# Performance work log

Hardware: AMD Instinct MI355X
Metric: run time of the kernel (lower is better)

Reference implementation:

```python
import jax, jax.numpy as jnp
import numpy as np

B, C, H, W = 1024, 3, 32, 32
NCLS = 10

def _conv(x, w, b, padding):
    y = jax.lax.conv_general_dilated(x, w, (1, 1), padding, dimension_numbers=('NCHW', 'OIHW', 'NCHW'))
    return y + b[None, :, None, None]

def _maxpool2(x):
    return jax.lax.reduce_window(x, -jnp.inf, jax.lax.max, (1, 1, 2, 2), (1, 1, 2, 2), 'VALID')

def _lenet(x, lw1, lb1, lw2, lb2, lfc1, lfb1, lfc2, lfb2, lfc3, lfb3):
    h = jax.nn.relu(_conv(x, lw1, lb1, 'VALID'))   # [B,6,28,28]
    h = _maxpool2(h)                               # [B,6,14,14]
    h = jax.nn.relu(_conv(h, lw2, lb2, 'VALID'))   # [B,16,10,10]
    h = _maxpool2(h)                               # [B,16,5,5]
    h = h.reshape(h.shape[0], -1)                  # [B,400]
    h = jax.nn.relu(h @ lfc1 + lfb1)
    h = jax.nn.relu(h @ lfc2 + lfb2)
    return h @ lfc3 + lfb3                         # [B,10]

def _resnet(x, rw0, rb0, rw1a, rb1a, rw1b, rb1b, rw2a, rb2a, rw2b, rb2b, rfc, rfb):
    h = jax.nn.relu(_conv(x, rw0, rb0, 'SAME'))    # [B,64,32,32]
    r = jax.nn.relu(_conv(h, rw1a, rb1a, 'SAME'))
    r = _conv(r, rw1b, rb1b, 'SAME')
    h = jax.nn.relu(h + r)
    r = jax.nn.relu(_conv(h, rw2a, rb2a, 'SAME'))
    r = _conv(r, rw2b, rb2b, 'SAME')
    h = jax.nn.relu(h + r)
    h = h.mean(axis=(2, 3))                        # [B,64]
    return h @ rfc + rfb                           # [B,10]

def setup_inputs():
    key = jax.random.key(0)
    ks = jax.random.split(key, 16)
    def w(k, shape, fan_in):
        return jax.random.normal(k, shape, jnp.float32) * np.float32(1.0 / np.sqrt(fan_in))
    return {
        'x': jax.random.normal(ks[0], (B, C, H, W), jnp.float32),
        'threshold': jnp.float32(0.3),
        'labels': jax.random.randint(ks[1], (B,), 0, NCLS),
        'lw1': w(ks[2], (6, 3, 5, 5), 75), 'lb1': jnp.zeros((6,), jnp.float32),
        'lw2': w(ks[3], (16, 6, 5, 5), 150), 'lb2': jnp.zeros((16,), jnp.float32),
        'lfc1': w(ks[4], (400, 120), 400), 'lfb1': jnp.zeros((120,), jnp.float32),
        'lfc2': w(ks[5], (120, 84), 120), 'lfb2': jnp.zeros((84,), jnp.float32),
        'lfc3': w(ks[6], (84, NCLS), 84), 'lfb3': jnp.zeros((NCLS,), jnp.float32),
        'rw0': w(ks[7], (64, 3, 3, 3), 27), 'rb0': jnp.zeros((64,), jnp.float32),
        'rw1a': w(ks[8], (64, 64, 3, 3), 576), 'rb1a': jnp.zeros((64,), jnp.float32),
        'rw1b': w(ks[9], (64, 64, 3, 3), 576), 'rb1b': jnp.zeros((64,), jnp.float32),
        'rw2a': w(ks[10], (64, 64, 3, 3), 576), 'rb2a': jnp.zeros((64,), jnp.float32),
        'rw2b': w(ks[11], (64, 64, 3, 3), 576), 'rb2b': jnp.zeros((64,), jnp.float32),
        'rfc': w(ks[12], (64, NCLS), 64), 'rfb': jnp.zeros((NCLS,), jnp.float32),
    }

def reference(x, threshold, labels, lw1, lb1, lw2, lb2, lfc1, lfb1, lfc2, lfb2, lfc3, lfb3, rw0, rb0, rw1a, rb1a, rw1b, rb1b, rw2a, rb2a, rw2b, rb2b, rfc, rfb):
    out = _lenet(x, lw1, lb1, lw2, lb2, lfc1, lfb1, lfc2, lfb2, lfc3, lfb3)
    pred = jnp.argmax(out, axis=1)
    # fused confusion-matrix update: single scatter-add replaces the 10x10 python loop
    conf_matrix = jnp.zeros((NCLS, NCLS), jnp.float32).at[labels, pred].add(1.0)
    probs = jax.nn.softmax(out, axis=1)
    top2, _ = jax.lax.top_k(probs, 2)
    low_conf = (top2[:, 0] - top2[:, 1]) <= threshold    # [B] bool
    # batched fallback: one grouped resnet call + masked merge replaces the per-sample loop
    res_out = _resnet(x, rw0, rb0, rw1a, rb1a, rw1b, rb1b, rw2a, rb2a, rw2b, rb2b, rfc, rfb)
    out = jnp.where(low_conf[:, None], res_out, out)
    return out, conf_matrix
```

## Files before the change

### kernel.cpp

```cpp
#include <hip/hip_runtime.h>
#include <hip/hip_bf16.h>
#include <math.h>

#define BATCH 1024

typedef __attribute__((ext_vector_type(8))) short bf16x8;
typedef __attribute__((ext_vector_type(4))) float f32x4;

#define IMG_ELEMS 73984
#define IMG_B 147968
#define ROW_B 4352
#define CH_B 544
#define WT_OFF 43520
#define WT_HALF_B 36864

__global__ __launch_bounds__(256) void lenet_conv1(const float* __restrict__ x,
    const float* __restrict__ w, const float* __restrict__ bias, float* __restrict__ p1)
{
    __shared__ float img[3 * 1024];
    __shared__ float wl[450];
    __shared__ float bl[6];
    int b = blockIdx.x, t = threadIdx.x;
    for (int i = t; i < 3072; i += 256) img[i] = x[(size_t)b * 3072 + i];
    for (int i = t; i < 450; i += 256) wl[i] = w[i];
    if (t < 6) bl[t] = bias[t];
    __syncthreads();
    for (int idx = t; idx < 1176; idx += 256) {
        int o = idx / 196, r = idx - o * 196, py = r / 14, px = r - py * 14;
        int y0 = 2 * py, x0 = 2 * px;
        float s00, s01, s10, s11;
        s00 = s01 = s10 = s11 = bl[o];
        for (int c = 0; c < 3; c++) {
            float pv[6][6];
            #pragma unroll
            for (int i2 = 0; i2 < 6; i2++)
                #pragma unroll
                for (int j2 = 0; j2 < 6; j2++)
                    pv[i2][j2] = img[c * 1024 + (y0 + i2) * 32 + x0 + j2];
            const float* wc = &wl[o * 75 + c * 25];
            #pragma unroll
            for (int ky = 0; ky < 5; ky++)
                #pragma unroll
                for (int kx = 0; kx < 5; kx++) {
                    float wv = wc[ky * 5 + kx];
                    s00 += pv[ky][kx] * wv;
                    s01 += pv[ky][kx + 1] * wv;
                    s10 += pv[ky + 1][kx] * wv;
                    s11 += pv[ky + 1][kx + 1] * wv;
                }
        }
        float m = fmaxf(fmaxf(s00, s01), fmaxf(s10, s11));
        p1[(size_t)b * 1176 + idx] = fmaxf(m, 0.f);
    }
}

__global__ __launch_bounds__(256) void lenet_conv2(const float* __restrict__ p1,
    const float* __restrict__ w, const float* __restrict__ bias, float* __restrict__ p2)
{
    __shared__ float img[1176];
    __shared__ float wl[2400];
    __shared__ float bl[16];
    int b = blockIdx.x, t = threadIdx.x;
    for (int i = t; i < 1176; i += 256) img[i] = p1[(size_t)b * 1176 + i];
    for (int i = t; i < 2400; i += 256) wl[i] = w[i];
    if (t < 16) bl[t] = bias[t];
    __syncthreads();
    for (int idx = t; idx < 400; idx += 256) {
        int o = idx / 25, r = idx - o * 25, py = r / 5, px = r - py * 5;
        int y0 = 2 * py, x0 = 2 * px;
        float s00, s01, s10, s11;
        s00 = s01 = s10 = s11 = bl[o];
        for (int c = 0; c < 6; c++) {
            float pv[6][6];
            #pragma unroll
            for (int i2 = 0; i2 < 6; i2++)
                #pragma unroll
                for (int j2 = 0; j2 < 6; j2++)
                    pv[i2][j2] = img[c * 196 + (y0 + i2) * 14 + x0 + j2];
            const float* wc = &wl[o * 150 + c * 25];
            #pragma unroll
            for (int ky = 0; ky < 5; ky++)
                #pragma unroll
                for (int kx = 0; kx < 5; kx++) {
                    float wv = wc[ky * 5 + kx];
                    s00 += pv[ky][kx] * wv;
                    s01 += pv[ky][kx + 1] * wv;
                    s10 += pv[ky + 1][kx] * wv;
                    s11 += pv[ky + 1][kx + 1] * wv;
                }
        }
        float m = fmaxf(fmaxf(s00, s01), fmaxf(s10, s11));
        p2[(size_t)b * 400 + idx] = fmaxf(m, 0.f);
    }
}

__global__ __launch_bounds__(256) void lenet_fc(const float* __restrict__ p2,
    const float* __restrict__ w1, const float* __restrict__ b1,
    const float* __restrict__ w2, const float* __restrict__ b2,
    const float* __restrict__ w3, const float* __restrict__ b3,
    const int* __restrict__ labels, const float* __restrict__ thr,
    float* __restrict__ out, float* __restrict__ conf, int* __restrict__ flags)
{
    __shared__ float xin[400];
    __shared__ float h1[120];
    __shared__ float h2[84];
    __shared__ float ps[256];
    __shared__ float lg[10];
    int b = blockIdx.x, t = threadIdx.x;
    for (int i = t; i < 400; i += 256) xin[i] = p2[(size_t)b * 400 + i];
    __syncthreads();
    {
        int n = t & 127, half = t >> 7;
        float s = 0.f;
        if (n < 120) {
            int k0 = half * 200;
            for (int k = k0; k < k0 + 200; k++) s += xin[k] * w1[k * 120 + n];
        }
        ps[t] = s;
    }
    __syncthreads();
    if (t < 120) h1[t] = fmaxf(ps[t] + ps[t + 128] + b1[t], 0.f);
    __syncthreads();
    {
        int n = t & 127, half = t >> 7;
        float s = 0.f;
        if (n < 84) {
            int k0 = half * 60;
            for (int k = k0; k < k0 + 60; k++) s += h1[k] * w2[k * 84 + n];
        }
        ps[t] = s;
    }
    __syncthreads();
    if (t < 84) h2[t] = fmaxf(ps[t] + ps[t + 128] + b2[t], 0.f);
    __syncthreads();
    if (t < 10) {
        float s = b3[t];
        for (int k = 0; k < 84; k++) s += h2[k] * w3[k * 10 + t];
        lg[t] = s;
        out[(size_t)b * 10 + t] = s;
    }
    __syncthreads();
    if (t == 0) {
        int pred = 0;
        float m = lg[0];
        #pragma unroll
        for (int j = 1; j < 10; j++) if (lg[j] > m) { m = lg[j]; pred = j; }
        float se = 0.f, m2 = -1e30f;
        #pragma unroll
        for (int j = 0; j < 10; j++) {
            se += expf(lg[j] - m);
            if (j != pred) m2 = fmaxf(m2, lg[j]);
        }
        float gap = (1.f - expf(m2 - m)) / se;
        flags[b] = (gap <= thr[0]) ? 1 : 0;
        atomicAdd(&conf[labels[b] * 10 + pred], 1.f);
    }
}

__global__ __launch_bounds__(256) void prep_weights(
    const float* __restrict__ w0, const float* __restrict__ w1,
    const float* __restrict__ w2, const float* __restrict__ w3,
    __hip_bfloat16* __restrict__ dst)
{
    int tid = blockIdx.x * 256 + threadIdx.x;
    if (tid >= 4 * 36864) return;
    int c = tid / 36864, r = tid - c * 36864;
    int tap = r / 4096, r2 = r - tap * 4096;
    int co = r2 >> 6, ci = r2 & 63;
    const float* src = (c == 0) ? w0 : (c == 1) ? w1 : (c == 2) ? w2 : w3;
    float v = src[((size_t)co * 64 + ci) * 9 + tap];
    int nh = co >> 5, nt = (co >> 4) & 1, m = co & 15;
    int kb = ci >> 5, q = (ci >> 3) & 3, e = ci & 7;
    size_t elem = (size_t)(c * 2 + nh) * 18432
                + (size_t)((tap * 2 + kb) * 2 + nt) * 512 + q * 128 + m * 8 + e;
    dst[elem] = __float2bfloat16(v);
}

__global__ __launch_bounds__(256) void prep_w0t(const float* __restrict__ w,
                                                float* __restrict__ dst)
{
    int tid = blockIdx.x * 256 + threadIdx.x;
    if (tid >= 1728) return;
    int k = tid >> 6, co = tid & 63;
    dst[tid] = w[co * 27 + k];
}

__global__ __launch_bounds__(256) void zero_borders(__hip_bfloat16* __restrict__ buf, int cb)
{
    int tid = blockIdx.x * 256 + threadIdx.x;
    int total = cb * 132 * 8;
    if (tid >= total) return;
    int img = tid / 1056, r = tid - img * 1056;
    int pxi = r >> 3, chunk = r & 7;
    int row, col;
    if (pxi < 34)       { row = 0;  col = pxi; }
    else if (pxi < 68)  { row = 33; col = pxi - 34; }
    else if (pxi < 100) { row = pxi - 67; col = 0; }
    else                { row = pxi - 99; col = 33; }
    uint4 z = {0, 0, 0, 0};
    *(uint4*)((char*)buf + (size_t)img * IMG_B + (size_t)row * ROW_B
              + chunk * CH_B + col * 16) = z;
}

__global__ __launch_bounds__(256) void conv0_nhwc(const float* __restrict__ x,
    const float* __restrict__ wT, const float* __restrict__ bias,
    __hip_bfloat16* __restrict__ out, int cb)
{
    __shared__ char smem[8 * ROW_B];
    float* sl = (float*)smem;
    int bid = blockIdx.x;
    int img = bid % cb, strip = bid / cb;
    int r0 = strip * 8;
    int t = threadIdx.x;
    const float* xi = x + (size_t)img * 3072;
    for (int i = t; i < 1020; i += 256) {
        int c = i / 340, rr2 = i - c * 340;
        int rr = rr2 / 34, cc = rr2 - rr * 34;
        int y = r0 + rr - 1, xx = cc - 1;
        float v = 0.f;
        if (y >= 0 && y < 32 && xx >= 0 && xx < 32) v = xi[c * 1024 + y * 32 + xx];
        sl[(c * 10 + rr) * 34 + cc] = v;
    }
    __syncthreads();

    int rr = t >> 5, col = t & 31;
    float iv[27];
    #pragma unroll
    for (int c = 0; c < 3; c++)
        #pragma unroll
        for (int dy = 0; dy < 3; dy++)
            #pragma unroll
            for (int dx = 0; dx < 3; dx++)
                iv[c * 9 + dy * 3 + dx] = sl[(c * 10 + rr + dy) * 34 + col + dx];
    __syncthreads();

    float s[64];
    #pragma unroll
    for (int co = 0; co < 64; co++) s[co] = bias[co];
    #pragma unroll
    for (int k = 0; k < 27; k++) {
        const float v = iv[k];
        const float* wk = wT + k * 64;
        #pragma unroll
        for (int co = 0; co < 64; co++) s[co] = fmaf(v, wk[co], s[co]);
    }
    __hip_bfloat16 ov[64];
    #pragma unroll
    for (int co = 0; co < 64; co++) ov[co] = __float2bfloat16(fmaxf(s[co], 0.f));

    char* brow = smem + rr * ROW_B + (col + 1) * 16;
    const uint4* srcv = (const uint4*)ov;
    #pragma unroll
    for (int j = 0; j < 8; j++) *(uint4*)(brow + j * CH_B) = srcv[j];
    if (t < 128) {
        int row = t >> 4, ch = (t >> 1) & 7, side = t & 1;
        uint4 z = {0, 0, 0, 0};
        *(uint4*)(smem + row * ROW_B + ch * CH_B + (side ? 33 : 0) * 16) = z;
    }
    __syncthreads();
    char* gbase = (char*)out + (size_t)img * IMG_B + (size_t)(r0 + 1) * ROW_B;
    for (int u = t; u < 2176; u += 256)
        *(uint4*)(gbase + (size_t)u * 16) = *(const uint4*)(smem + (size_t)u * 16);
}

template<bool ADD>
__global__ __launch_bounds__(256, 2) void conv3x3_lds(
    const __hip_bfloat16* __restrict__ act, const __hip_bfloat16* __restrict__ wts,
    const float* __restrict__ bias, const __hip_bfloat16* __restrict__ skip,
    __hip_bfloat16* __restrict__ out, int cb)
{
    __shared__ char sl[WT_OFF + WT_HALF_B];
    int bid = blockIdx.x;
    int img = bid % cb;
    int rem = bid / cb;
    int strip = rem >> 1, nh = rem & 1;
    int t = threadIdx.x;
    int w = t >> 6, lane = t & 63;
    int m = lane & 15, q = lane >> 4;

    const char* gsrc = (const char*)act + (size_t)img * IMG_B + (size_t)(strip * 8) * ROW_B;
    for (int u0 = w * 64; u0 < 2720; u0 += 256) {
        int u = u0 + lane;
        if (u < 2720)
            __builtin_amdgcn_global_load_lds(
                (const __attribute__((address_space(1))) unsigned int*)(gsrc + (size_t)u * 16),
                (__attribute__((address_space(3))) unsigned int*)(sl + u0 * 16), 16, 0, 0);
    }
    const char* gw = (const char*)wts + (size_t)nh * WT_HALF_B;
    for (int u0 = w * 64; u0 < 2304; u0 += 256)
        __builtin_amdgcn_global_load_lds(
            (const __attribute__((address_space(1))) unsigned int*)(gw + (size_t)(u0 + lane) * 16),
            (__attribute__((address_space(3))) unsigned int*)(sl + WT_OFF + u0 * 16), 16, 0, 0);
    __syncthreads();

    int abase[4];
    #pragma unroll
    for (int mt = 0; mt < 4; mt++)
        abase[mt] = (2 * w + (mt >> 1)) * ROW_B + ((mt & 1) * 16 + m) * 16 + q * CH_B;
    int bbase[2];
    #pragma unroll
    for (int nt = 0; nt < 2; nt++)
        bbase[nt] = WT_OFF + nt * 1024 + q * 256 + m * 16;

    f32x4 acc[4][2] = {};
    bf16x8 a[2][4], b[2][2];

    #define ALOAD(s, buf)                                                      \
        {                                                                      \
            const int tap_ = (s) >> 1, kb_ = (s) & 1;                          \
            const int dy_ = tap_ / 3, dx_ = tap_ - dy_ * 3;                    \
            const int aoff_ = dy_ * ROW_B + kb_ * (4 * CH_B) + dx_ * 16;       \
            _Pragma("unroll")                                                  \
            for (int mt = 0; mt < 4; mt++)                                     \
                a[buf][mt] = *(const bf16x8*)(sl + abase[mt] + aoff_);         \
        }
    #define BLOAD(s, buf)                                                      \
        {                                                                      \
            const int boff_ = ((s) >> 1) * 4096 + ((s) & 1) * 2048;            \
            _Pragma("unroll")                                                  \
            for (int nt = 0; nt < 2; nt++)                                     \
                b[buf][nt] = *(const bf16x8*)(sl + bbase[nt] + boff_);         \
        }

    ALOAD(0, 0) BLOAD(0, 0)
    #pragma unroll
    for (int s = 0; s < 18; s++) {
        int cur = s & 1;
        if (s < 17) { ALOAD(s + 1, cur ^ 1) BLOAD(s + 1, cur ^ 1) }
        #pragma unroll
        for (int mt = 0; mt < 4; mt++)
            #pragma unroll
            for (int nt = 0; nt < 2; nt++)
                acc[mt][nt] = __builtin_amdgcn_mfma_f32_16x16x32_bf16(
                    a[cur][mt], b[cur][nt], acc[mt][nt], 0, 0, 0);
    }
    #undef ALOAD
    #undef BLOAD

    __syncthreads();
    #pragma unroll
    for (int nt = 0; nt < 2; nt++) {
        float bv = bias[nh * 32 + nt * 16 + m];
        #pragma unroll
        for (int mt = 0; mt < 4; mt++) {
            int pl = (2 * w + (mt >> 1)) * 32 + (mt & 1) * 16 + q * 4;
            #pragma unroll
            for (int r = 0; r < 4; r++) {
                __hip_bfloat16 hv = __float2bfloat16(acc[mt][nt][r] + bv);
                *(__hip_bfloat16*)(sl + (size_t)(pl + r) * 72 + (nt * 16 + m) * 2) = hv;
            }
        }
    }
    __syncthreads();

    char* oimg = (char*)out + (size_t)img * IMG_B;
    const char* simg = (const char*)skip + (size_t)img * IMG_B;
    int ch = (t >> 5) & 3, px = t & 31, rhalf = t >> 7;
    #pragma unroll
    for (int pass = 0; pass < 4; pass++) {
        int rl = pass * 2 + rhalf;
        size_t goff = (size_t)(strip * 8 + 1 + rl) * ROW_B + (nh * 4 + ch) * CH_B + (px + 1) * 16;
        bf16x8 v = *(const bf16x8*)(sl + (size_t)(rl * 32 + px) * 72 + ch * 16);
        bf16x8 o;
        if (ADD) {
            bf16x8 sv = *(const bf16x8*)(simg + goff);
            #pragma unroll
            for (int e = 0; e < 8; e++) {
                float f = __bfloat162float(((__hip_bfloat16*)&v)[e])
                        + __bfloat162float(((__hip_bfloat16*)&sv)[e]);
                ((__hip_bfloat16*)&o)[e] = __float2bfloat16(fmaxf(f, 0.f));
            }
        } else {
            #pragma unroll
            for (int e = 0; e < 8; e++) {
                float f = __bfloat162float(((__hip_bfloat16*)&v)[e]);
                ((__hip_bfloat16*)&o)[e] = __float2bfloat16(fmaxf(f, 0.f));
            }
        }
        *(bf16x8*)(oimg + goff) = o;
    }
}

__global__ __launch_bounds__(256) void res_head_bf16(const __hip_bfloat16* __restrict__ h,
    const float* __restrict__ rfc, const float* __restrict__ rfb,
    const int* __restrict__ flags, float* __restrict__ out)
{
    __shared__ float part[4][64];
    __shared__ float mns[64];
    int img = blockIdx.x, t = threadIdx.x;
    int w = t >> 6, lane = t & 63;
    int c = lane & 7;
    const char* base = (const char*)h + (size_t)img * IMG_B;

    float s8[8];
    #pragma unroll
    for (int j = 0; j < 8; j++) s8[j] = 0.f;

    for (int ry = 0; ry < 8; ry++) {
        int row = w * 8 + ry + 1;
        const char* rb = base + (size_t)row * ROW_B;
        #pragma unroll
        for (int k = 0; k < 4; k++) {
            int g = lane + 64 * k;
            bf16x8 v = *(const bf16x8*)(rb + c * CH_B + ((g >> 3) + 1) * 16);
            #pragma unroll
            for (int j = 0; j < 8; j++)
                s8[j] += __bfloat162float(*(__hip_bfloat16*)&((short*)&v)[j]);
        }
    }
    #pragma unroll
    for (int off = 8; off <= 32; off <<= 1)
        #pragma unroll
        for (int j = 0; j < 8; j++) s8[j] += __shfl_xor(s8[j], off, 64);
    if (lane < 8)
        #pragma unroll
        for (int j = 0; j < 8; j++) part[w][c * 8 + j] = s8[j];
    __syncthreads();
    if (t < 64) mns[t] = (part[0][t] + part[1][t] + part[2][t] + part[3][t]) * (1.f / 1024.f);
    __syncthreads();
    if (t < 10 && flags[img]) {
        float s2 = rfb[t];
        for (int cc = 0; cc < 64; cc++) s2 += mns[cc] * rfc[cc * 10 + t];
        out[(size_t)img * 10 + t] = s2;
    }
}

extern "C" void kernel_launch(void* const* d_in, const int* in_sizes, int n_in,
                              void* d_out, int out_size, void* d_ws, size_t ws_size,
                              hipStream_t stream)
{
    const float* x    = (const float*)d_in[0];
    const float* thr  = (const float*)d_in[1];
    const int*   labels = (const int*)d_in[2];
    const float* lw1 = (const float*)d_in[3];  const float* lb1 = (const float*)d_in[4];
    const float* lw2 = (const float*)d_in[5];  const float* lb2 = (const float*)d_in[6];
    const float* lfc1 = (const float*)d_in[7]; const float* lfb1 = (const float*)d_in[8];
    const float* lfc2 = (const float*)d_in[9]; const float* lfb2 = (const float*)d_in[10];
    const float* lfc3 = (const float*)d_in[11];const float* lfb3 = (const float*)d_in[12];
    const float* rw0 = (const float*)d_in[13]; const float* rb0 = (const float*)d_in[14];
    const float* rw1a = (const float*)d_in[15];const float* rb1a = (const float*)d_in[16];
    const float* rw1b = (const float*)d_in[17];const float* rb1b = (const float*)d_in[18];
    const float* rw2a = (const float*)d_in[19];const float* rb2a = (const float*)d_in[20];
    const float* rw2b = (const float*)d_in[21];const float* rb2b = (const float*)d_in[22];
    const float* rfc = (const float*)d_in[23]; const float* rfb = (const float*)d_in[24];

    float* out  = (float*)d_out;
    float* conf = out + (size_t)BATCH * 10;

    int nc = 1;
    while (nc < 16 &&
           2ull * (size_t)(BATCH / nc) * 147968ull + 294912ull + 16384ull > ws_size)
        nc <<= 1;
    int cb = BATCH / nc;

    __hip_bfloat16* A  = (__hip_bfloat16*)d_ws;
    __hip_bfloat16* Bb = A + (size_t)cb * IMG_ELEMS;
    __hip_bfloat16* wprep = Bb + (size_t)cb * IMG_ELEMS;
    int* flags = (int*)((char*)wprep + 294912);
    float* w0t = (float*)((char*)wprep + 294912 + 4096);

    float* p1 = (float*)A;
    float* p2 = p1 + 1204224;

    hipMemsetAsync(conf, 0, 100 * sizeof(float), stream);

    prep_weights<<<(4 * 36864 + 255) / 256, 256, 0, stream>>>(rw1a, rw1b, rw2a, rw2b, wprep);
    prep_w0t<<<7, 256, 0, stream>>>(rw0, w0t);

    lenet_conv1<<<BATCH, 256, 0, stream>>>(x, lw1, lb1, p1);
    lenet_conv2<<<BATCH, 256, 0, stream>>>(p1, lw2, lb2, p2);
    lenet_fc<<<BATCH, 256, 0, stream>>>(p2, lfc1, lfb1, lfc2, lfb2, lfc3, lfb3,
                                        labels, thr, out, conf, flags);

    int zb = (cb * 1056 + 255) / 256;
    zero_borders<<<zb, 256, 0, stream>>>(A, cb);
    zero_borders<<<zb, 256, 0, stream>>>(Bb, cb);

    const __hip_bfloat16* W1a = wprep;
    const __hip_bfloat16* W1b = wprep + 36864;
    const __hip_bfloat16* W2a = wprep + 2 * 36864;
    const __hip_bfloat16* W2b = wprep + 3 * 36864;

    for (int c0 = 0; c0 < BATCH; c0 += cb) {
        const float* xc = x + (size_t)c0 * 3072;
        conv0_nhwc<<<cb * 4, 256, 0, stream>>>(xc, w0t, rb0, A, cb);
        conv3x3_lds<false><<<cb * 8, 256, 0, stream>>>(A,  W1a, rb1a, nullptr, Bb, cb);
        conv3x3_lds<true ><<<cb * 8, 256, 0, stream>>>(Bb, W1b, rb1b, A, A, cb);
        conv3x3_lds<false><<<cb * 8, 256, 0, stream>>>(A,  W2a, rb2a, nullptr, Bb, cb);
        conv3x3_lds<true ><<<cb * 8, 256, 0, stream>>>(Bb, W2b, rb2b, A, A, cb);
        res_head_bf16<<<cb, 256, 0, stream>>>(A, rfc, rfb, flags + c0, out + (size_t)c0 * 10);
    }
}
```

Before: 702.9 us.

## Make conv3x3 blocks persistent over four row strips with prefetched halo

```diff
diff --git a/kernel.cpp b/kernel.cpp
--- a/kernel.cpp
+++ b/kernel.cpp
@@ -13,6 +13,8 @@
 #define CH_B 544
 #define WT_OFF 43520
 #define WT_HALF_B 36864
+#define BOUNCE_OFF 25088
+#define STAGE_A_U 1568
 
 __global__ __launch_bounds__(256) void lenet_conv1(const float* __restrict__ x,
     const float* __restrict__ w, const float* __restrict__ bias, float* __restrict__ p1)
@@ -263,6 +265,11 @@
         *(uint4*)(gbase + (size_t)u * 16) = *(const uint4*)(smem + (size_t)u * 16);
 }
 
+#define GLL(gp, lp)                                                            \
+    __builtin_amdgcn_global_load_lds(                                          \
+        (const __attribute__((address_space(1))) unsigned int*)(gp),           \
+        (__attribute__((address_space(3))) unsigned int*)(lp), 16, 0, 0)
+
 template<bool ADD>
 __global__ __launch_bounds__(256, 2) void conv3x3_lds(
     const __hip_bfloat16* __restrict__ act, const __hip_bfloat16* __restrict__ wts,
@@ -271,27 +278,22 @@
 {
     __shared__ char sl[WT_OFF + WT_HALF_B];
     int bid = blockIdx.x;
-    int img = bid % cb;
-    int rem = bid / cb;
-    int strip = rem >> 1, nh = rem & 1;
+    int img = bid % cb, nh = bid / cb;
     int t = threadIdx.x;
     int w = t >> 6, lane = t & 63;
     int m = lane & 15, q = lane >> 4;
 
-    const char* gsrc = (const char*)act + (size_t)img * IMG_B + (size_t)(strip * 8) * ROW_B;
+    const char* gimg = (const char*)act + (size_t)img * IMG_B;
+
+    const char* gw = (const char*)wts + (size_t)nh * WT_HALF_B;
+    for (int u0 = w * 64; u0 < 2304; u0 += 256)
+        GLL(gw + (size_t)(u0 + lane) * 16, sl + WT_OFF + u0 * 16);
     for (int u0 = w * 64; u0 < 2720; u0 += 256) {
         int u = u0 + lane;
-        if (u < 2720)
-            __builtin_amdgcn_global_load_lds(
-                (const __attribute__((address_space(1))) unsigned int*)(gsrc + (size_t)u * 16),
-                (__attribute__((address_space(3))) unsigned int*)(sl + u0 * 16), 16, 0, 0);
-    }
-    const char* gw = (const char*)wts + (size_t)nh * WT_HALF_B;
-    for (int u0 = w * 64; u0 < 2304; u0 += 256)
-        __builtin_amdgcn_global_load_lds(
-            (const __attribute__((address_space(1))) unsigned int*)(gw + (size_t)(u0 + lane) * 16),
-            (__attribute__((address_space(3))) unsigned int*)(sl + WT_OFF + u0 * 16), 16, 0, 0);
-    __syncthreads();
+        if (u < 2720) GLL(gimg + (size_t)u * 16, sl + u0 * 16);
+    }
+    asm volatile("s_waitcnt vmcnt(0)" ::: "memory");
+    __builtin_amdgcn_s_barrier();
 
     int abase[4];
     #pragma unroll
@@ -301,83 +303,110 @@
     #pragma unroll
     for (int nt = 0; nt < 2; nt++)
         bbase[nt] = WT_OFF + nt * 1024 + q * 256 + m * 16;
-
-    f32x4 acc[4][2] = {};
-    bf16x8 a[2][4], b[2][2];
-
-    #define ALOAD(s, buf)                                                      \
-        {                                                                      \
-            const int tap_ = (s) >> 1, kb_ = (s) & 1;                          \
-            const int dy_ = tap_ / 3, dx_ = tap_ - dy_ * 3;                    \
-            const int aoff_ = dy_ * ROW_B + kb_ * (4 * CH_B) + dx_ * 16;       \
-            _Pragma("unroll")                                                  \
-            for (int mt = 0; mt < 4; mt++)                                     \
-                a[buf][mt] = *(const bf16x8*)(sl + abase[mt] + aoff_);         \
-        }
-    #define BLOAD(s, buf)                                                      \
-        {                                                                      \
-            const int boff_ = ((s) >> 1) * 4096 + ((s) & 1) * 2048;            \
-            _Pragma("unroll")                                                  \
-            for (int nt = 0; nt < 2; nt++)                                     \
-                b[buf][nt] = *(const bf16x8*)(sl + bbase[nt] + boff_);         \
-        }
-
-    ALOAD(0, 0) BLOAD(0, 0)
-    #pragma unroll
-    for (int s = 0; s < 18; s++) {
-        int cur = s & 1;
-        if (s < 17) { ALOAD(s + 1, cur ^ 1) BLOAD(s + 1, cur ^ 1) }
-        #pragma unroll
-        for (int mt = 0; mt < 4; mt++)
-            #pragma unroll
-            for (int nt = 0; nt < 2; nt++)
-                acc[mt][nt] = __builtin_amdgcn_mfma_f32_16x16x32_bf16(
-                    a[cur][mt], b[cur][nt], acc[mt][nt], 0, 0, 0);
-    }
-    #undef ALOAD
-    #undef BLOAD
-
-    __syncthreads();
-    #pragma unroll
-    for (int nt = 0; nt < 2; nt++) {
-        float bv = bias[nh * 32 + nt * 16 + m];
-        #pragma unroll
-        for (int mt = 0; mt < 4; mt++) {
-            int pl = (2 * w + (mt >> 1)) * 32 + (mt & 1) * 16 + q * 4;
-            #pragma unroll
-            for (int r = 0; r < 4; r++) {
-                __hip_bfloat16 hv = __float2bfloat16(acc[mt][nt][r] + bv);
-                *(__hip_bfloat16*)(sl + (size_t)(pl + r) * 72 + (nt * 16 + m) * 2) = hv;
+    float bv[2] = { bias[nh * 32 + m], bias[nh * 32 + 16 + m] };
+
+    for (int strip = 0; strip < 4; ++strip) {
+        f32x4 acc[4][2] = {};
+        bf16x8 a[2][4], b[2][2];
+
+        #define ALOAD(s, buf)                                                  \
+            {                                                                  \
+                const int tap_ = (s) >> 1, kb_ = (s) & 1;                      \
+                const int dy_ = tap_ / 3, dx_ = tap_ - dy_ * 3;                \
+                const int aoff_ = dy_ * ROW_B + kb_ * (4 * CH_B) + dx_ * 16;   \
+                _Pragma("unroll")                                              \
+                for (int mt = 0; mt < 4; mt++)                                 \
+                    a[buf][mt] = *(const bf16x8*)(sl + abase[mt] + aoff_);     \
             }
-        }
-    }
-    __syncthreads();
-
-    char* oimg = (char*)out + (size_t)img * IMG_B;
-    const char* simg = (const char*)skip + (size_t)img * IMG_B;
-    int ch = (t >> 5) & 3, px = t & 31, rhalf = t >> 7;
-    #pragma unroll
-    for (int pass = 0; pass < 4; pass++) {
-        int rl = pass * 2 + rhalf;
-        size_t goff = (size_t)(strip * 8 + 1 + rl) * ROW_B + (nh * 4 + ch) * CH_B + (px + 1) * 16;
-        bf16x8 v = *(const bf16x8*)(sl + (size_t)(rl * 32 + px) * 72 + ch * 16);
-        bf16x8 o;
-        if (ADD) {
-            bf16x8 sv = *(const bf16x8*)(simg + goff);
-            #pragma unroll
-            for (int e = 0; e < 8; e++) {
-                float f = __bfloat162float(((__hip_bfloat16*)&v)[e])
-                        + __bfloat162float(((__hip_bfloat16*)&sv)[e]);
-                ((__hip_bfloat16*)&o)[e] = __float2bfloat16(fmaxf(f, 0.f));
+        #define BLOAD(s, buf)                                                  \
+            {                                                                  \
+                const int boff_ = ((s) >> 1) * 4096 + ((s) & 1) * 2048;        \
+                _Pragma("unroll")                                              \
+                for (int nt = 0; nt < 2; nt++)                                 \
+                    b[buf][nt] = *(const bf16x8*)(sl + bbase[nt] + boff_);     \
             }
-        } else {
-            #pragma unroll
-            for (int e = 0; e < 8; e++) {
-                float f = __bfloat162float(((__hip_bfloat16*)&v)[e]);
-                ((__hip_bfloat16*)&o)[e] = __float2bfloat16(fmaxf(f, 0.f));
+
+        ALOAD(0, 0) BLOAD(0, 0)
+        #pragma unroll
+        for (int s = 0; s < 18; s++) {
+            int cur = s & 1;
+            if (s < 17) { ALOAD(s + 1, cur ^ 1) BLOAD(s + 1, cur ^ 1) }
+            #pragma unroll
+            for (int mt = 0; mt < 4; mt++)
+                #pragma unroll
+                for (int nt = 0; nt < 2; nt++)
+                    acc[mt][nt] = __builtin_amdgcn_mfma_f32_16x16x32_bf16(
+                        a[cur][mt], b[cur][nt], acc[mt][nt], 0, 0, 0);
+        }
+        #undef ALOAD
+        #undef BLOAD
+
+        asm volatile("s_waitcnt lgkmcnt(0)" ::: "memory");
+        __builtin_amdgcn_s_barrier();
+        const char* gn = gimg + (size_t)(strip + 1) * (8 * ROW_B);
+        if (strip < 3)
+            for (int u0 = w * 64; u0 < STAGE_A_U; u0 += 256) {
+                int u = u0 + lane;
+                if (u < STAGE_A_U) GLL(gn + (size_t)u * 16, sl + u0 * 16);
             }
-        }
-        *(bf16x8*)(oimg + goff) = o;
+
+        #pragma unroll
+        for (int nt = 0; nt < 2; nt++) {
+            #pragma unroll
+            for (int mt = 0; mt < 4; mt++) {
+                int pl = (2 * w + (mt >> 1)) * 32 + (mt & 1) * 16 + q * 4;
+                #pragma unroll
+                for (int r = 0; r < 4; r++) {
+                    __hip_bfloat16 hv = __float2bfloat16(acc[mt][nt][r] + bv[nt]);
+                    *(__hip_bfloat16*)(sl + BOUNCE_OFF + (size_t)(pl + r) * 72
+                                       + (nt * 16 + m) * 2) = hv;
+                }
+            }
+        }
+        asm volatile("s_waitcnt lgkmcnt(0)" ::: "memory");
+        __builtin_amdgcn_s_barrier();
+
+        {
+            char* oimg = (char*)out + (size_t)img * IMG_B;
+            const char* simg = (const char*)skip + (size_t)img * IMG_B;
+            int ch = (t >> 5) & 3, px = t & 31, rhalf = t >> 7;
+            #pragma unroll
+            for (int pass = 0; pass < 4; pass++) {
+                int rl = pass * 2 + rhalf;
+                size_t goff = (size_t)(strip * 8 + 1 + rl) * ROW_B
+                            + (nh * 4 + ch) * CH_B + (px + 1) * 16;
+                bf16x8 v = *(const bf16x8*)(sl + BOUNCE_OFF
+                            + (size_t)(rl * 32 + px) * 72 + ch * 16);
+                bf16x8 o;
+                if (ADD) {
+                    bf16x8 sv = *(const bf16x8*)(simg + goff);
+                    #pragma unroll
+                    for (int e = 0; e < 8; e++) {
+                        float f = __bfloat162float(((__hip_bfloat16*)&v)[e])
+                                + __bfloat162float(((__hip_bfloat16*)&sv)[e]);
+                        ((__hip_bfloat16*)&o)[e] = __float2bfloat16(fmaxf(f, 0.f));
+                    }
+                } else {
+                    #pragma unroll
+                    for (int e = 0; e < 8; e++) {
+                        float f = __bfloat162float(((__hip_bfloat16*)&v)[e]);
+                        ((__hip_bfloat16*)&o)[e] = __float2bfloat16(fmaxf(f, 0.f));
+                    }
+                }
+                *(bf16x8*)(oimg + goff) = o;
+            }
+        }
+
+        if (strip < 3) {
+            asm volatile("s_waitcnt lgkmcnt(0)" ::: "memory");
+            __builtin_amdgcn_s_barrier();
+            for (int u0 = STAGE_A_U + w * 64; u0 < 2720; u0 += 256) {
+                int u = u0 + lane;
+                if (u < 2720) GLL(gn + (size_t)u * 16, sl + u0 * 16);
+            }
+            asm volatile("s_waitcnt vmcnt(0)" ::: "memory");
+            __builtin_amdgcn_s_barrier();
+        }
     }
 }
 
@@ -484,10 +513,10 @@
     for (int c0 = 0; c0 < BATCH; c0 += cb) {
         const float* xc = x + (size_t)c0 * 3072;
         conv0_nhwc<<<cb * 4, 256, 0, stream>>>(xc, w0t, rb0, A, cb);
-        conv3x3_lds<false><<<cb * 8, 256, 0, stream>>>(A,  W1a, rb1a, nullptr, Bb, cb);
-        conv3x3_lds<true ><<<cb * 8, 256, 0, stream>>>(Bb, W1b, rb1b, A, A, cb);
-        conv3x3_lds<false><<<cb * 8, 256, 0, stream>>>(A,  W2a, rb2a, nullptr, Bb, cb);
-        conv3x3_lds<true ><<<cb * 8, 256, 0, stream>>>(Bb, W2b, rb2b, A, A, cb);
+        conv3x3_lds<false><<<cb * 2, 256, 0, stream>>>(A,  W1a, rb1a, nullptr, Bb, cb);
+        conv3x3_lds<true ><<<cb * 2, 256, 0, stream>>>(Bb, W1b, rb1b, A, A, cb);
+        conv3x3_lds<false><<<cb * 2, 256, 0, stream>>>(A,  W2a, rb2a, nullptr, Bb, cb);
+        conv3x3_lds<true ><<<cb * 2, 256, 0, stream>>>(Bb, W2b, rb2b, A, A, cb);
         res_head_bf16<<<cb, 256, 0, stream>>>(A, rfc, rfb, flags + c0, out + (size_t)c0 * 10);
     }
 }
```

After: 713.5 us. Within noise of the previous version (+1.5%).
